# Kernel optimization log

Measured on AMD Instinct MI355X. Metric: run time of the kernel, lower is better.

Reference implementation:

```python
import jax, jax.numpy as jnp
import numpy as np

TAU = 1.0

def setup_inputs() -> dict:
    key = jax.random.key(0)
    scores = jax.random.normal(key, (16, 2048), dtype=jnp.float32)
    return {"scores": scores}

def reference(scores):
    # scores: [B, n]
    B, n = scores.shape
    # row-sum of pairwise abs differences: Asum[b,i] = sum_k |s_i - s_k|
    Asum = jnp.sum(jnp.abs(scores[:, :, None] - scores[:, None, :]), axis=-1)  # [B, n]
    # scaling[j] = n + 1 - 2*(j+1)
    scaling = (n + 1 - 2 * (jnp.arange(n, dtype=jnp.float32) + 1.0))  # [n]
    # P_max[b, j, i] = s[b,i] * scaling[j] - Asum[b,i]
    P_max = scores[:, None, :] * scaling[None, :, None] - Asum[:, None, :]  # [B, n, n]
    P_hat = jax.nn.softmax(P_max / TAU, axis=-1)
    return P_hat
```

## Files before the change

### kernel.cpp

```cpp
#include <hip/hip_runtime.h>
#include <hip/hip_bf16.h>

#define N 2048
#define B 16

typedef float v4f __attribute__((ext_vector_type(4)));

__global__ __launch_bounds__(256) void asum_kernel(const float* __restrict__ s,
                                                   float* __restrict__ asum) {
    const int b = blockIdx.y;
    const int i = blockIdx.x * 256 + threadIdx.x;

    __shared__ float row[N];
    const v4f* g4 = (const v4f*)(s + b * N);
    v4f* r4 = (v4f*)row;
    r4[threadIdx.x] = g4[threadIdx.x];
    r4[threadIdx.x + 256] = g4[threadIdx.x + 256];
    __syncthreads();

    const float si = row[i];
    const v4f* row4 = (const v4f*)row;
    float acc = 0.0f;
#pragma unroll 4
    for (int k = 0; k < N / 4; ++k) {
        v4f rv = row4[k];
        acc += fabsf(si - rv.x) + fabsf(si - rv.y) +
               fabsf(si - rv.z) + fabsf(si - rv.w);
    }
    asum[b * N + i] = acc;
}

__global__ __launch_bounds__(256) void softmax_rows(const float* __restrict__ s,
                                                    const float* __restrict__ asum,
                                                    float* __restrict__ out) {
    const int t = threadIdx.x;
    const int lane = t & 63;
    const int wave = t >> 6;
    const int j = blockIdx.x * 4 + wave;
    const int b = blockIdx.y;

    const float cj = (float)(N - 1 - 2 * j);

    const v4f* s4 = (const v4f*)(s + (size_t)b * N);
    const v4f* a4 = (const v4f*)(asum + (size_t)b * N);

    float v[32];
#pragma unroll
    for (int c = 0; c < 8; ++c) {
        v4f sv = s4[c * 64 + lane];
        v4f av = a4[c * 64 + lane];
        v[c * 4 + 0] = sv.x * cj - av.x;
        v[c * 4 + 1] = sv.y * cj - av.y;
        v[c * 4 + 2] = sv.z * cj - av.z;
        v[c * 4 + 3] = sv.w * cj - av.w;
    }

    float m = v[0];
#pragma unroll
    for (int i = 1; i < 32; ++i) m = fmaxf(m, v[i]);
#pragma unroll
    for (int off = 32; off >= 1; off >>= 1)
        m = fmaxf(m, __shfl_xor(m, off));

    float sum = 0.0f;
#pragma unroll
    for (int i = 0; i < 32; ++i) {
        v[i] = __expf(v[i] - m);
        sum += v[i];
    }
#pragma unroll
    for (int off = 32; off >= 1; off >>= 1)
        sum += __shfl_xor(sum, off);

    const float r = 1.0f / sum;

    v4f* o4 = (v4f*)(out + ((size_t)b * N + j) * N);
#pragma unroll
    for (int c = 0; c < 8; ++c) {
        v4f o;
        o.x = v[c * 4 + 0] * r;
        o.y = v[c * 4 + 1] * r;
        o.z = v[c * 4 + 2] * r;
        o.w = v[c * 4 + 3] * r;
        __builtin_nontemporal_store(o, &o4[c * 64 + lane]);
    }
}

extern "C" void kernel_launch(void* const* d_in, const int* in_sizes, int n_in,
                              void* d_out, int out_size, void* d_ws, size_t ws_size,
                              hipStream_t stream) {
    const float* scores = (const float*)d_in[0];
    float* out = (float*)d_out;
    float* asum = (float*)d_ws;

    dim3 g1(N / 256, B);
    asum_kernel<<<g1, 256, 0, stream>>>(scores, asum);

    dim3 g2(N / 4, B);
    softmax_rows<<<g2, 256, 0, stream>>>(scores, asum, out);
}
```

Before: 279.2 us.

## Split softmax into row-stats pass and grid-strided streaming write kernel

The asum kernel now splits each row's reduction across two half-blocks and combines the partials through shared memory, doubling the block count. The fused softmax is split in two. A row-stats kernel computes each row's max and reciprocal sum. A separate grid-strided kernel then recomputes the exponentials and streams the 256 MB output with nontemporal stores. This is meant to get a more uniform, bandwidth-friendly write pattern. The cost is an extra launch and computing the exp twice.

After: 295.9 us. 1.06x slower.

```diff
diff --git a/kernel.cpp b/kernel.cpp
--- a/kernel.cpp
+++ b/kernel.cpp
@@ -5,34 +5,42 @@
 #define B 16
 
 typedef float v4f __attribute__((ext_vector_type(4)));
+typedef float v2f __attribute__((ext_vector_type(2)));
 
 __global__ __launch_bounds__(256) void asum_kernel(const float* __restrict__ s,
                                                    float* __restrict__ asum) {
     const int b = blockIdx.y;
-    const int i = blockIdx.x * 256 + threadIdx.x;
+    const int chunk = blockIdx.x;
 
     __shared__ float row[N];
+    __shared__ float partial[256];
     const v4f* g4 = (const v4f*)(s + b * N);
     v4f* r4 = (v4f*)row;
     r4[threadIdx.x] = g4[threadIdx.x];
     r4[threadIdx.x + 256] = g4[threadIdx.x + 256];
     __syncthreads();
 
+    const int il = threadIdx.x & 127;
+    const int half = threadIdx.x >> 7;
+    const int i = chunk * 128 + il;
     const float si = row[i];
-    const v4f* row4 = (const v4f*)row;
+    const v4f* row4 = (const v4f*)(row + half * (N / 2));
     float acc = 0.0f;
 #pragma unroll 4
-    for (int k = 0; k < N / 4; ++k) {
+    for (int k = 0; k < N / 8; ++k) {
         v4f rv = row4[k];
         acc += fabsf(si - rv.x) + fabsf(si - rv.y) +
                fabsf(si - rv.z) + fabsf(si - rv.w);
     }
-    asum[b * N + i] = acc;
+    partial[threadIdx.x] = acc;
+    __syncthreads();
+    if (threadIdx.x < 128)
+        asum[b * N + i] = partial[threadIdx.x] + partial[threadIdx.x + 128];
 }
 
-__global__ __launch_bounds__(256) void softmax_rows(const float* __restrict__ s,
-                                                    const float* __restrict__ asum,
-                                                    float* __restrict__ out) {
+__global__ __launch_bounds__(256) void rowstats_kernel(const float* __restrict__ s,
+                                                       const float* __restrict__ asum,
+                                                       v2f* __restrict__ mz) {
     const int t = threadIdx.x;
     const int lane = t & 63;
     const int wave = t >> 6;
@@ -64,25 +72,49 @@
 
     float sum = 0.0f;
 #pragma unroll
-    for (int i = 0; i < 32; ++i) {
-        v[i] = __expf(v[i] - m);
-        sum += v[i];
-    }
+    for (int i = 0; i < 32; ++i)
+        sum += __expf(v[i] - m);
 #pragma unroll
     for (int off = 32; off >= 1; off >>= 1)
         sum += __shfl_xor(sum, off);
 
-    const float r = 1.0f / sum;
+    if (lane == 0) {
+        v2f r;
+        r.x = m;
+        r.y = 1.0f / sum;
+        mz[(size_t)b * N + j] = r;
+    }
+}
 
-    v4f* o4 = (v4f*)(out + ((size_t)b * N + j) * N);
+#define STREAM_BLOCKS 8192
+__global__ __launch_bounds__(256) void stream_kernel(const float* __restrict__ s,
+                                                     const float* __restrict__ asum,
+                                                     const v2f* __restrict__ mz,
+                                                     float* __restrict__ out) {
+    const int tid = blockIdx.x * 256 + threadIdx.x;
+    const int nth = STREAM_BLOCKS * 256;
+    v4f* o4 = (v4f*)out;
 #pragma unroll
-    for (int c = 0; c < 8; ++c) {
+    for (int it = 0; it < 8; ++it) {
+        const int c = tid + it * nth;
+        const int i4 = c & (N / 4 - 1);
+        const int row = c >> 9;
+        const int j = row & (N - 1);
+        const int b = row >> 11;
+
+        const v4f sv = ((const v4f*)(s + b * N))[i4];
+        const v4f av = ((const v4f*)(asum + b * N))[i4];
+        const v2f mr = mz[row];
+        const float cj = (float)(N - 1 - 2 * j);
+        const float mm = mr.x;
+        const float rz = mr.y;
+
         v4f o;
-        o.x = v[c * 4 + 0] * r;
-        o.y = v[c * 4 + 1] * r;
-        o.z = v[c * 4 + 2] * r;
-        o.w = v[c * 4 + 3] * r;
-        __builtin_nontemporal_store(o, &o4[c * 64 + lane]);
+        o.x = __expf(sv.x * cj - av.x - mm) * rz;
+        o.y = __expf(sv.y * cj - av.y - mm) * rz;
+        o.z = __expf(sv.z * cj - av.z - mm) * rz;
+        o.w = __expf(sv.w * cj - av.w - mm) * rz;
+        __builtin_nontemporal_store(o, &o4[c]);
     }
 }
 
@@ -92,10 +124,13 @@
     const float* scores = (const float*)d_in[0];
     float* out = (float*)d_out;
     float* asum = (float*)d_ws;
+    v2f* mz = (v2f*)((char*)d_ws + B * N * 4);
 
-    dim3 g1(N / 256, B);
+    dim3 g1(N / 128, B);
     asum_kernel<<<g1, 256, 0, stream>>>(scores, asum);
 
     dim3 g2(N / 4, B);
-    softmax_rows<<<g2, 256, 0, stream>>>(scores, asum, out);
+    rowstats_kernel<<<g2, 256, 0, stream>>>(scores, asum, mz);
+
+    stream_kernel<<<STREAM_BLOCKS, 256, 0, stream>>>(scores, asum, mz, out);
 }
```
